# Kernel tuning notes

Measured on AMD Instinct MI355X. Metric: run time of the kernel, lower is better.

## Reference

```python
import math
import jax, jax.numpy as jnp
import numpy as np

B, C, L, EMB, ORDER = 4, 768, 8192, 33, 64


def setup_inputs() -> dict:
    key = jax.random.key(0)
    ks = jax.random.split(key, 8)
    x = jax.random.normal(ks[0], (B, C, L), jnp.float32)
    # 'batchias' param: jax.nn.initializers.normal() -> stddev 1e-2
    bias = 0.01 * jax.random.normal(ks[1], (C,), jnp.float32)
    # PositionalEmbedding z param (deterministic init)
    bands = (EMB - 1) // 2
    t_rescaled = jnp.linspace(0, L - 1, L)[None, :, None]
    w = 2 * math.pi * t_rescaled / L
    f = jnp.linspace(1e-4, bands - 1, bands)[None, None]
    zc = jnp.exp(-1j * f * w)
    time_emb = jnp.linspace(0, 1, L)[None, :, None]
    z = jnp.concatenate([time_emb, zc.real, zc.imag], axis=2).astype(jnp.float32)
    # ExponentialModulation deltas (deterministic init)
    target, fast_decay_pct, slow_decay_pct = 0.01, 0.3, 1.5
    max_decay = math.log(target) / fast_decay_pct
    min_decay = math.log(target) / slow_decay_pct
    deltas = jnp.linspace(min_decay, max_decay, C)[None, None].astype(jnp.float32)
    # implicit filter MLP params (Dense default lecun_normal-ish scale)
    def dense(k, fi, fo):
        return (jax.random.normal(k, (fi, fo), jnp.float32) / np.float32(np.sqrt(fi)))
    W0 = dense(ks[2], EMB, ORDER); b0 = jnp.zeros((ORDER,), jnp.float32)
    W1 = dense(ks[3], ORDER, ORDER); b1 = jnp.zeros((ORDER,), jnp.float32)
    W2 = dense(ks[4], ORDER, ORDER); b2 = jnp.zeros((ORDER,), jnp.float32)
    Wout = dense(ks[5], ORDER, C)  # no bias
    # Sin act constructed as Sin(dim=order) -> default freq=10, shared instance
    freq = 10.0 * jnp.ones((1, ORDER), jnp.float32)
    return dict(x=x, bias=bias, z=z, deltas=deltas, W0=W0, b0=b0, W1=W1, b1=b1,
                W2=W2, b2=b2, freq=freq, Wout=Wout, seq_len=L)


def _filter(z, deltas, W0, b0, W1, b1, W2, b2, freq, Wout, seq_len):
    # implicit MLP: (Dense -> Sin) x3, then Dense(num_channels, no bias)
    h = jnp.sin(freq * (z @ W0 + b0))
    h = jnp.sin(freq * (h @ W1 + b1))
    h = jnp.sin(freq * (h @ W2 + b2))
    h = h @ Wout  # [1, L, C]
    # exponential modulation: t = linspace(0,1,seq_len)
    t = jnp.linspace(0, 1, seq_len)[None, :, None]
    h = h * jnp.exp(-t * jnp.abs(deltas))
    return h


def _fft_conv(u, k, D):
    # u: [B, C, L], k: [C, L], D: [C]
    seq_len = u.shape[-1]
    fft_size = 2 * seq_len
    k_f = jnp.fft.rfft(k, n=fft_size) / fft_size
    u_f = jnp.fft.rfft(u, n=fft_size)
    y = jnp.fft.irfft(u_f * k_f, n=fft_size, norm='forward')[..., :seq_len]
    return (y + u * D[:, None]).astype(u.dtype)


def reference(x, bias, z, deltas, W0, b0, W1, b1, W2, b2, freq, Wout, seq_len):
    h = _filter(z, deltas, W0, b0, W1, b1, W2, b2, freq, Wout, seq_len)  # [1, L, C]
    k = h[0].T  # [C, L] (channel-major kernel as consumed by fft_conv)
    return _fft_conv(x, k, bias)
```

## Files before the change

### kernel.cpp

```cpp
#include <hip/hip_runtime.h>
#include <type_traits>
#include <utility>


typedef __attribute__((ext_vector_type(4))) short  short4v;
typedef __attribute__((ext_vector_type(8))) short  short8v;
typedef __attribute__((ext_vector_type(8))) __bf16 bf16x8;
typedef __attribute__((ext_vector_type(16))) float f32x16;

template <typename V, typename = void> struct MfmaTakes : std::false_type {};
template <typename V>
struct MfmaTakes<V, std::void_t<decltype(__builtin_amdgcn_mfma_f32_32x32x16_bf16(
    std::declval<V>(), std::declval<V>(), std::declval<f32x16>(), 0, 0, 0))>>
    : std::true_type {};

template <bool UseBf16> struct MfmaImpl;
template <> struct MfmaImpl<true> {
  template <typename V>
  static __device__ inline f32x16 run(V a, V b, f32x16 c) {
    return __builtin_amdgcn_mfma_f32_32x32x16_bf16(
        __builtin_bit_cast(bf16x8, a), __builtin_bit_cast(bf16x8, b), c, 0, 0, 0);
  }
};
template <> struct MfmaImpl<false> {
  template <typename V>
  static __device__ inline f32x16 run(V a, V b, f32x16 c) {
    return __builtin_amdgcn_mfma_f32_32x32x16_bf16(a, b, c, 0, 0, 0);
  }
};

__device__ inline f32x16 mfma_bf16(short8v a, short8v b, f32x16 c) {
  return MfmaImpl<MfmaTakes<bf16x8>::value>::run(a, b, c);
}

__device__ inline short8v pack8(short4v lo, short4v hi) {
  short8v v;
  v[0] = lo[0]; v[1] = lo[1]; v[2] = lo[2]; v[3] = lo[3];
  v[4] = hi[0]; v[5] = hi[1]; v[6] = hi[2]; v[7] = hi[3];
  return v;
}

__device__ inline short f2bf(float f) {
  unsigned int u = __builtin_bit_cast(unsigned int, f);
  u += 0x7FFFu + ((u >> 16) & 1u);
  return (short)(u >> 16);
}
__device__ inline float bf2f(short s) {
  unsigned int u = ((unsigned int)(unsigned short)s) << 16;
  return __builtin_bit_cast(float, u);
}

__device__ const unsigned char cGt[16]  = {2,7,4,6,1,7,4,6,5,7,3,6,3,0,5,5};
__device__ const short         cN0[16]  = {0,0,0,0,0,86,80,75,0,171,64,150,0,0,64,128};
__device__ const short         cN1[16]  = {96,86,80,75,64,171,160,150,64,256,128,224,64,32,128,192};
__device__ const unsigned char cSLOT[16]= {255,255,255,255,255,0,1,2,255,3,4,5,255,255,6,7};
__device__ const unsigned char cRA[16]  = {255,0,1,2,255,255,255,255,6,255,255,255,4,255,255,255};
__device__ const unsigned char cRB[16]  = {255,3,255,5,255,255,255,255,7,255,255,255,255,255,255,255};

__global__ __launch_bounds__(256) void hyena_filter(
    const float* __restrict__ z, const float* __restrict__ deltas,
    const float* __restrict__ W0, const float* __restrict__ b0,
    const float* __restrict__ W1, const float* __restrict__ b1,
    const float* __restrict__ W2, const float* __restrict__ b2,
    const float* __restrict__ freq, const float* __restrict__ Wout,
    short* __restrict__ gk) {
  __shared__ float zt[32][33];
  __shared__ __align__(16) float hA[32][64];
  __shared__ __align__(16) float hB[32][64];
  __shared__ __align__(16) unsigned int sT[256][20];
  const int tid = threadIdx.x;
  const int l0 = blockIdx.x << 5;

  for (int i = tid; i < 32 * 33; i += 256) {
    int l = i / 33, e = i - l * 33;
    zt[l][e] = z[(l0 + l) * 33 + e];
  }
  __syncthreads();
  for (int i = tid; i < 2048; i += 256) {
    int l = i >> 6, o = i & 63;
    float s = b0[o];
    for (int e = 0; e < 33; ++e) s += zt[l][e] * W0[e * 64 + o];
    hA[l][o] = sinf(freq[o] * s);
  }
  __syncthreads();
  for (int i = tid; i < 2048; i += 256) {
    int l = i >> 6, o = i & 63;
    float s = b1[o];
#pragma unroll
    for (int e = 0; e < 64; e += 4) {
      const float4 h4 = *reinterpret_cast<const float4*>(&hA[l][e]);
      s += h4.x * W1[e * 64 + o] + h4.y * W1[(e + 1) * 64 + o] +
           h4.z * W1[(e + 2) * 64 + o] + h4.w * W1[(e + 3) * 64 + o];
    }
    hB[l][o] = sinf(freq[o] * s);
  }
  __syncthreads();
  for (int i = tid; i < 2048; i += 256) {
    int l = i >> 6, o = i & 63;
    float s = b2[o];
#pragma unroll
    for (int e = 0; e < 64; e += 4) {
      const float4 h4 = *reinterpret_cast<const float4*>(&hB[l][e]);
      s += h4.x * W2[e * 64 + o] + h4.y * W2[(e + 1) * 64 + o] +
           h4.z * W2[(e + 2) * 64 + o] + h4.w * W2[(e + 3) * 64 + o];
    }
    hA[l][o] = sinf(freq[o] * s);
  }
  __syncthreads();
  {
    const int c0 = (blockIdx.y << 8) + tid;
    float a32[32];
#pragma unroll
    for (int l = 0; l < 32; ++l) a32[l] = 0.f;
    for (int o = 0; o < 64; o += 4) {
      const float w0 = Wout[(o + 0) * 768 + c0];
      const float w1 = Wout[(o + 1) * 768 + c0];
      const float w2 = Wout[(o + 2) * 768 + c0];
      const float w3 = Wout[(o + 3) * 768 + c0];
#pragma unroll
      for (int l = 0; l < 32; ++l) {
        const float4 h4 = *reinterpret_cast<const float4*>(&hA[l][o]);
        a32[l] += h4.x * w0 + h4.y * w1 + h4.z * w2 + h4.w * w3;
      }
    }
    const float del = fabsf(deltas[c0]);
#pragma unroll
    for (int l = 0; l < 32; ++l) {
      const float t = (float)(l0 + l) * (1.f / 8191.f);
      a32[l] *= expf(-t * del);
    }
#pragma unroll
    for (int d = 0; d < 16; ++d) {
      const unsigned int lo = (unsigned short)f2bf(a32[31 - 2 * d]);
      const unsigned int hi = (unsigned short)f2bf(a32[30 - 2 * d]);
      sT[tid][d] = lo | (hi << 16);
    }
  }
  __syncthreads();
  {
    const int lane = tid & 63, wid = tid >> 6;
    const int base_dw = 4080 - (blockIdx.x << 4);
    unsigned int* gku = reinterpret_cast<unsigned int*>(gk);
#pragma unroll
    for (int q = 0; q < 4; ++q) {
      const int r = (wid << 6) + (q << 4) + (lane >> 2);
      const int m = (lane & 3) << 2;
      const uint4 v = *reinterpret_cast<const uint4*>(&sT[r][m]);
      const size_t cg = (size_t)((blockIdx.y << 8) + r);
      *reinterpret_cast<uint4*>(gku + cg * 4096 + base_dw + m) = v;
    }
  }
}


#define ACC_ST(ACC, P, OFF)                                           \
  do {                                                                \
    _Pragma("unroll") for (int q = 0; q < 4; ++q) {                   \
      float4 v;                                                       \
      v.x = ACC[4 * q + 0]; v.y = ACC[4 * q + 1];                     \
      v.z = ACC[4 * q + 2]; v.w = ACC[4 * q + 3];                     \
      *reinterpret_cast<float4*>((P) + (OFF) + (q << 8)) = v;         \
    }                                                                 \
  } while (0)

#define ACC_LD(ACC, P, OFF)                                           \
  do {                                                                \
    _Pragma("unroll") for (int q = 0; q < 4; ++q) {                   \
      const float4 v =                                                \
          *reinterpret_cast<const float4*>((P) + (OFF) + (q << 8));   \
      ACC[4 * q + 0] += v.x; ACC[4 * q + 1] += v.y;                   \
      ACC[4 * q + 2] += v.z; ACC[4 * q + 3] += v.w;                   \
    }                                                                 \
  } while (0)

#define EPI(ACC, A)                                                   \
  do {                                                                \
    const int lb = lwb + ((A) << 8);                                  \
    _Pragma("unroll") for (int q = 0; q < 4; ++q) {                   \
      const int l0q = lb + (q << 3);                                  \
      const short4v xs =                                              \
          *reinterpret_cast<const short4v*>(&sXB[bcol][1008 + l0q]);  \
      float4 o4;                                                      \
      o4.x = ACC[4 * q + 0] + bc * bf2f(xs[0]);                       \
      o4.y = ACC[4 * q + 1] + bc * bf2f(xs[1]);                       \
      o4.z = ACC[4 * q + 2] + bc * bf2f(xs[2]);                       \
      o4.w = ACC[4 * q + 3] + bc * bf2f(xs[3]);                       \
      *reinterpret_cast<float4*>(out + obase + l0q) = o4;             \
    }                                                                 \
  } while (0)

__global__ __launch_bounds__(1024, 4) void hyena_conv(
    const float* __restrict__ x, const float* __restrict__ bias,
    const short* __restrict__ gk, float* __restrict__ out) {
  constexpr int LPAD = 1008;
  constexpr int XROW = 9224;
  __shared__ __align__(16) short sKR[4][8240];
  __shared__ __align__(16) short sXB[4][XROW];
  const int c = blockIdx.x;
  const int tid = threadIdx.x;

  {
    const short8v z8 = {0, 0, 0, 0, 0, 0, 0, 0};
    for (int b = 0; b < 4; ++b) {
      const float* xr = x + ((b * 768 + c) << 13);
      if (tid < 126)
        *reinterpret_cast<short8v*>(&sXB[b][tid << 3]) = z8;
      if (tid >= 1021)
        *reinterpret_cast<short8v*>(&sXB[b][9200 + ((tid - 1021) << 3)]) = z8;
      const int s0 = tid << 3;
      const float4 f0 = *reinterpret_cast<const float4*>(xr + s0);
      const float4 f1 = *reinterpret_cast<const float4*>(xr + s0 + 4);
      short8v v;
      v[0] = f2bf(f0.x); v[1] = f2bf(f0.y); v[2] = f2bf(f0.z); v[3] = f2bf(f0.w);
      v[4] = f2bf(f1.x); v[5] = f2bf(f1.y); v[6] = f2bf(f1.z); v[7] = f2bf(f1.w);
      *reinterpret_cast<short8v*>(&sXB[b][LPAD + s0]) = v;
    }
  }
  {
    const short* gkr = gk + (c << 13);
    for (int r = 0; r < 4; ++r)
      for (int u = tid; u < 8240; u += 1024) {
        int t = u + r;
        short v = 0;
        if (t >= 16 && t <= 8207) v = gkr[t - 16];
        sKR[r][u] = v;
      }
  }
  __syncthreads();

  const int lane = tid & 63;
  const int wid  = tid >> 6;
  const int i31  = lane & 31;
  const int half = lane >> 5;
  const int base = half << 3;
  const int tcol = i31 >> 2;
  const int bcol = i31 & 3;
  const float bc = bias[c];

  const int G    = cGt[wid];
  const int n0   = cN0[wid];
  const int n1   = cN1[wid];
  const int slot = cSLOT[wid];
  const int lbase = G << 10;

  const int af0 = 8207 - i31 + base;
  const int rho = af0 & 3;
  const int u00 = af0 & ~3;
  const int pb  = LPAD + lbase + (tcol << 5) + base;
  const int d0  = ((n0 >> 4) << 9) + ((n0 & 15) << 4);

  const short* ka = &sKR[rho][0] + (u00 + 16 - d0);
  const short* xa = &sXB[bcol][0] + (pb + 16 - d0);

  f32x16 acc0, acc1, acc2, acc3;
#pragma unroll
  for (int r = 0; r < 16; ++r) {
    acc0[r] = 0.f; acc1[r] = 0.f; acc2[r] = 0.f; acc3[r] = 0.f;
  }

#pragma unroll 2
  for (int n = n0; n < n1; ++n) {
    const short4v a0lo = *reinterpret_cast<const short4v*>(ka);
    const short4v a0hi = *reinterpret_cast<const short4v*>(ka + 4);
    const short4v a1lo = *reinterpret_cast<const short4v*>(ka - 256);
    const short4v a1hi = *reinterpret_cast<const short4v*>(ka - 252);
    const short8v A0 = pack8(a0lo, a0hi);
    const short8v A1 = pack8(a1lo, a1hi);
    const short8v Bm1 = *reinterpret_cast<const short8v*>(xa - 256);
    const short8v B0  = *reinterpret_cast<const short8v*>(xa);
    acc0 = mfma_bf16(A1, Bm1, acc0);
    acc0 = mfma_bf16(A0, B0, acc0);
    const short8v B1 = *reinterpret_cast<const short8v*>(xa + 256);
    acc1 = mfma_bf16(A1, B0, acc1);
    acc1 = mfma_bf16(A0, B1, acc1);
    const short8v B2 = *reinterpret_cast<const short8v*>(xa + 512);
    acc2 = mfma_bf16(A1, B1, acc2);
    acc2 = mfma_bf16(A0, B2, acc2);
    const short8v B3 = *reinterpret_cast<const short8v*>(xa + 768);
    acc3 = mfma_bf16(A1, B2, acc3);
    acc3 = mfma_bf16(A0, B3, acc3);
    const int dec = 16 + (((n & 15) == 15) << 8);
    ka -= dec; xa -= dec;
  }

  __syncthreads();
  float* scr = reinterpret_cast<float*>(&sKR[0][0]);
  const int isOwner = (slot == 255);
  float* sp = scr + (isOwner ? 0 : slot * 2048) + (lane << 2);
  const int ra = cRA[wid], rb = cRB[wid];
  if (!isOwner) { ACC_ST(acc0, sp, 0); ACC_ST(acc1, sp, 1024); }
  __syncthreads();
  if (isOwner) {
    if (ra != 255) {
      float* lp = scr + ra * 2048 + (lane << 2);
      ACC_LD(acc0, lp, 0); ACC_LD(acc1, lp, 1024);
    }
    if (rb != 255) {
      float* lp = scr + rb * 2048 + (lane << 2);
      ACC_LD(acc0, lp, 0); ACC_LD(acc1, lp, 1024);
    }
  }
  __syncthreads();
  if (!isOwner) { ACC_ST(acc2, sp, 0); ACC_ST(acc3, sp, 1024); }
  __syncthreads();
  if (isOwner) {
    if (ra != 255) {
      float* lp = scr + ra * 2048 + (lane << 2);
      ACC_LD(acc2, lp, 0); ACC_LD(acc3, lp, 1024);
    }
    if (rb != 255) {
      float* lp = scr + rb * 2048 + (lane << 2);
      ACC_LD(acc2, lp, 0); ACC_LD(acc3, lp, 1024);
    }
    const int obase = ((bcol * 768 + c) << 13);
    const int lwb = lbase + (tcol << 5) + (half << 2);
    EPI(acc0, 0); EPI(acc1, 1); EPI(acc2, 2); EPI(acc3, 3);
  }
}

extern "C" void kernel_launch(void* const* d_in, const int* in_sizes, int n_in,
                              void* d_out, int out_size, void* d_ws, size_t ws_size,
                              hipStream_t stream) {
  const float* x      = (const float*)d_in[0];
  const float* bias   = (const float*)d_in[1];
  const float* z      = (const float*)d_in[2];
  const float* deltas = (const float*)d_in[3];
  const float* W0     = (const float*)d_in[4];
  const float* b0     = (const float*)d_in[5];
  const float* W1     = (const float*)d_in[6];
  const float* b1     = (const float*)d_in[7];
  const float* W2     = (const float*)d_in[8];
  const float* b2     = (const float*)d_in[9];
  const float* freq   = (const float*)d_in[10];
  const float* Wout   = (const float*)d_in[11];
  float* out = (float*)d_out;
  short* gk = (short*)d_ws;

  hipLaunchKernelGGL(hyena_filter, dim3(256, 3), dim3(256), 0, stream,
                     z, deltas, W0, b0, W1, b1, W2, b2, freq, Wout, gk);
  hipLaunchKernelGGL(hyena_conv, dim3(768), dim3(1024), 0, stream,
                     x, bias, gk, out);
}
```

Before: 407.1 us.

## Split filter into MLP and Wout kernels; reorder conv MFMAs with setprio

The single filter kernel is split in two. One kernel computes the sine MLP once per position into a workspace buffer, and a second does the Wout projection with exponential modulation, writing the reversed bf16 kernel. This stops the MLP from being recomputed for each of the three channel groups and spreads the projection over more blocks. The conv inner loop now hoists all B loads ahead of the MFMAs, groups them by A operand and raises wave priority around them. The cost is an extra launch plus a global round trip for the hidden activations, and the new path only runs when the workspace is large enough.

```diff
diff --git a/kernel.cpp b/kernel.cpp
--- a/kernel.cpp
+++ b/kernel.cpp
@@ -57,7 +57,99 @@
 __device__ const unsigned char cRA[16]  = {255,0,1,2,255,255,255,255,6,255,255,255,4,255,255,255};
 __device__ const unsigned char cRB[16]  = {255,3,255,5,255,255,255,255,7,255,255,255,255,255,255,255};
 
-__global__ __launch_bounds__(256) void hyena_filter(
+__global__ __launch_bounds__(256) void hyena_mlp(
+    const float* __restrict__ z,
+    const float* __restrict__ W0, const float* __restrict__ b0,
+    const float* __restrict__ W1, const float* __restrict__ b1,
+    const float* __restrict__ W2, const float* __restrict__ b2,
+    const float* __restrict__ freq, float* __restrict__ h) {
+  __shared__ float zt[32][33];
+  __shared__ __align__(16) float hA[32][64];
+  __shared__ __align__(16) float hB[32][64];
+  const int tid = threadIdx.x;
+  const int l0 = blockIdx.x << 5;
+
+  for (int i = tid; i < 32 * 33; i += 256) {
+    int l = i / 33, e = i - l * 33;
+    zt[l][e] = z[(l0 + l) * 33 + e];
+  }
+  __syncthreads();
+  for (int i = tid; i < 2048; i += 256) {
+    int l = i >> 6, o = i & 63;
+    float s = b0[o];
+    for (int e = 0; e < 33; ++e) s += zt[l][e] * W0[e * 64 + o];
+    hA[l][o] = sinf(freq[o] * s);
+  }
+  __syncthreads();
+  for (int i = tid; i < 2048; i += 256) {
+    int l = i >> 6, o = i & 63;
+    float s = b1[o];
+#pragma unroll
+    for (int e = 0; e < 64; e += 4) {
+      const float4 h4 = *reinterpret_cast<const float4*>(&hA[l][e]);
+      s += h4.x * W1[e * 64 + o] + h4.y * W1[(e + 1) * 64 + o] +
+           h4.z * W1[(e + 2) * 64 + o] + h4.w * W1[(e + 3) * 64 + o];
+    }
+    hB[l][o] = sinf(freq[o] * s);
+  }
+  __syncthreads();
+  for (int i = tid; i < 2048; i += 256) {
+    int l = i >> 6, o = i & 63;
+    float s = b2[o];
+#pragma unroll
+    for (int e = 0; e < 64; e += 4) {
+      const float4 h4 = *reinterpret_cast<const float4*>(&hB[l][e]);
+      s += h4.x * W2[e * 64 + o] + h4.y * W2[(e + 1) * 64 + o] +
+           h4.z * W2[(e + 2) * 64 + o] + h4.w * W2[(e + 3) * 64 + o];
+    }
+    hA[l][o] = sinf(freq[o] * s);
+  }
+  __syncthreads();
+  for (int i = tid; i < 512; i += 256) {
+    const int l = i >> 4, o4 = (i & 15) << 2;
+    *reinterpret_cast<float4*>(h + ((l0 + l) << 6) + o4) =
+        *reinterpret_cast<const float4*>(&hA[l][o4]);
+  }
+}
+
+__global__ __launch_bounds__(256) void hyena_wout(
+    const float* __restrict__ h, const float* __restrict__ deltas,
+    const float* __restrict__ Wout, short* __restrict__ gk) {
+  const int tid = threadIdx.x;
+  const int c0 = (blockIdx.y << 8) + tid;
+  const int l0 = blockIdx.x << 4;
+  float a[16];
+#pragma unroll
+  for (int j = 0; j < 16; ++j) a[j] = 0.f;
+
+  const float* hb = h + ((size_t)l0 << 6);
+  for (int o = 0; o < 64; o += 4) {
+    const float w0 = Wout[(o + 0) * 768 + c0];
+    const float w1 = Wout[(o + 1) * 768 + c0];
+    const float w2 = Wout[(o + 2) * 768 + c0];
+    const float w3 = Wout[(o + 3) * 768 + c0];
+#pragma unroll
+    for (int j = 0; j < 16; ++j) {
+      const int off = __builtin_amdgcn_readfirstlane((j << 6) + o);
+      const float4 h4 = *reinterpret_cast<const float4*>(hb + off);
+      a[j] += h4.x * w0 + h4.y * w1 + h4.z * w2 + h4.w * w3;
+    }
+  }
+  const float del = fabsf(deltas[c0]);
+#pragma unroll
+  for (int j = 0; j < 16; ++j)
+    a[j] *= expf(-(float)(l0 + j) * (1.f / 8191.f) * del);
+
+  unsigned int* gku = reinterpret_cast<unsigned int*>(gk + ((size_t)c0 << 13));
+#pragma unroll
+  for (int j = 0; j < 16; j += 2) {
+    const unsigned int hi = (unsigned short)f2bf(a[j]);
+    const unsigned int lo = (unsigned short)f2bf(a[j + 1]);
+    gku[(8190 - l0 - j) >> 1] = lo | (hi << 16);
+  }
+}
+
+__global__ __launch_bounds__(256) void hyena_filter_mono(
     const float* __restrict__ z, const float* __restrict__ deltas,
     const float* __restrict__ W0, const float* __restrict__ b0,
     const float* __restrict__ W1, const float* __restrict__ b1,
@@ -268,17 +360,19 @@
     const short8v A1 = pack8(a1lo, a1hi);
     const short8v Bm1 = *reinterpret_cast<const short8v*>(xa - 256);
     const short8v B0  = *reinterpret_cast<const short8v*>(xa);
+    const short8v B1  = *reinterpret_cast<const short8v*>(xa + 256);
+    const short8v B2  = *reinterpret_cast<const short8v*>(xa + 512);
+    const short8v B3  = *reinterpret_cast<const short8v*>(xa + 768);
+    __builtin_amdgcn_s_setprio(1);
     acc0 = mfma_bf16(A1, Bm1, acc0);
+    acc1 = mfma_bf16(A1, B0, acc1);
+    acc2 = mfma_bf16(A1, B1, acc2);
+    acc3 = mfma_bf16(A1, B2, acc3);
     acc0 = mfma_bf16(A0, B0, acc0);
-    const short8v B1 = *reinterpret_cast<const short8v*>(xa + 256);
-    acc1 = mfma_bf16(A1, B0, acc1);
     acc1 = mfma_bf16(A0, B1, acc1);
-    const short8v B2 = *reinterpret_cast<const short8v*>(xa + 512);
-    acc2 = mfma_bf16(A1, B1, acc2);
     acc2 = mfma_bf16(A0, B2, acc2);
-    const short8v B3 = *reinterpret_cast<const short8v*>(xa + 768);
-    acc3 = mfma_bf16(A1, B2, acc3);
     acc3 = mfma_bf16(A0, B3, acc3);
+    __builtin_amdgcn_s_setprio(0);
     const int dec = 16 + (((n & 15) == 15) << 8);
     ka -= dec; xa -= dec;
   }
@@ -335,9 +429,19 @@
   const float* Wout   = (const float*)d_in[11];
   float* out = (float*)d_out;
   short* gk = (short*)d_ws;
-
-  hipLaunchKernelGGL(hyena_filter, dim3(256, 3), dim3(256), 0, stream,
-                     z, deltas, W0, b0, W1, b1, W2, b2, freq, Wout, gk);
+  const size_t GK_BYTES = (size_t)768 * 8192 * 2;
+  const size_t H_BYTES  = (size_t)8192 * 64 * 4;
+
+  if (ws_size >= GK_BYTES + H_BYTES) {
+    float* hbuf = (float*)((char*)d_ws + GK_BYTES);
+    hipLaunchKernelGGL(hyena_mlp, dim3(256), dim3(256), 0, stream,
+                       z, W0, b0, W1, b1, W2, b2, freq, hbuf);
+    hipLaunchKernelGGL(hyena_wout, dim3(512, 3), dim3(256), 0, stream,
+                       hbuf, deltas, Wout, gk);
+  } else {
+    hipLaunchKernelGGL(hyena_filter_mono, dim3(256, 3), dim3(256), 0, stream,
+                       z, deltas, W0, b0, W1, b1, W2, b2, freq, Wout, gk);
+  }
   hipLaunchKernelGGL(hyena_conv, dim3(768), dim3(1024), 0, stream,
                      x, bias, gk, out);
 }
```

After: 420.8 us. 3.3% more time.

## Widen conv MFMA inner step to four A fragments and shrink filter tiles

Applied to the files above, without the earlier changes.

The convolution inner loop now loads four kernel fragments (A0..A3) per step and issues sixteen MFMAs against shifted x fragments. It advances by 1024 per block of 16 steps instead of 512, so each warp takes fewer outer iterations with more register reuse of the loaded operands. The per-warp work-split tables are rebalanced for the new step size. The filter kernel now handles 16 positions per block over twice as many blocks and writes bf16 pairs straight to global memory, dropping the shared-memory transpose stage. That direct write pattern is less coalesced, and the wider loop raises register pressure.

```diff
diff --git a/kernel.cpp b/kernel.cpp
--- a/kernel.cpp
+++ b/kernel.cpp
@@ -50,12 +50,12 @@
   return __builtin_bit_cast(float, u);
 }
 
-__device__ const unsigned char cGt[16]  = {2,7,4,6,1,7,4,6,5,7,3,6,3,0,5,5};
-__device__ const short         cN0[16]  = {0,0,0,0,0,86,80,75,0,171,64,150,0,0,64,128};
-__device__ const short         cN1[16]  = {96,86,80,75,64,171,160,150,64,256,128,224,64,32,128,192};
-__device__ const unsigned char cSLOT[16]= {255,255,255,255,255,0,1,2,255,3,4,5,255,255,6,7};
-__device__ const unsigned char cRA[16]  = {255,0,1,2,255,255,255,255,6,255,255,255,4,255,255,255};
-__device__ const unsigned char cRB[16]  = {255,3,255,5,255,255,255,255,7,255,255,255,255,255,255,255};
+__device__ const unsigned char cGt[16]  = {0,1,2,3,7,3,5,6,7,4,5,6,7,4,5,6};
+__device__ const short         cN0[16]  = {0,0,0,0,0,32,0,0,43,0,32,38,86,40,64,75};
+__device__ const short         cN1[16]  = {16,32,48,32,43,64,32,38,86,40,64,75,128,80,96,112};
+__device__ const unsigned char cSLOT[16]= {255,255,255,255,255,0,255,255,1,255,2,3,4,5,6,7};
+__device__ const unsigned char cRA[16]  = {255,255,255,0,1,255,2,3,255,5,255,255,255,255,255,255};
+__device__ const unsigned char cRB[16]  = {255,255,255,255,4,255,6,7,255,255,255,255,255,255,255,255};
 
 __global__ __launch_bounds__(256) void hyena_filter(
     const float* __restrict__ z, const float* __restrict__ deltas,
@@ -64,26 +64,25 @@
     const float* __restrict__ W2, const float* __restrict__ b2,
     const float* __restrict__ freq, const float* __restrict__ Wout,
     short* __restrict__ gk) {
-  __shared__ float zt[32][33];
-  __shared__ __align__(16) float hA[32][64];
-  __shared__ __align__(16) float hB[32][64];
-  __shared__ __align__(16) unsigned int sT[256][20];
+  __shared__ float zt[16][33];
+  __shared__ __align__(16) float hA[16][64];
+  __shared__ __align__(16) float hB[16][64];
   const int tid = threadIdx.x;
-  const int l0 = blockIdx.x << 5;
-
-  for (int i = tid; i < 32 * 33; i += 256) {
+  const int l0 = blockIdx.x << 4;
+
+  for (int i = tid; i < 16 * 33; i += 256) {
     int l = i / 33, e = i - l * 33;
     zt[l][e] = z[(l0 + l) * 33 + e];
   }
   __syncthreads();
-  for (int i = tid; i < 2048; i += 256) {
+  for (int i = tid; i < 1024; i += 256) {
     int l = i >> 6, o = i & 63;
     float s = b0[o];
     for (int e = 0; e < 33; ++e) s += zt[l][e] * W0[e * 64 + o];
     hA[l][o] = sinf(freq[o] * s);
   }
   __syncthreads();
-  for (int i = tid; i < 2048; i += 256) {
+  for (int i = tid; i < 1024; i += 256) {
     int l = i >> 6, o = i & 63;
     float s = b1[o];
 #pragma unroll
@@ -95,7 +94,7 @@
     hB[l][o] = sinf(freq[o] * s);
   }
   __syncthreads();
-  for (int i = tid; i < 2048; i += 256) {
+  for (int i = tid; i < 1024; i += 256) {
     int l = i >> 6, o = i & 63;
     float s = b2[o];
 #pragma unroll
@@ -109,45 +108,31 @@
   __syncthreads();
   {
     const int c0 = (blockIdx.y << 8) + tid;
-    float a32[32];
-#pragma unroll
-    for (int l = 0; l < 32; ++l) a32[l] = 0.f;
+    float a[16];
+#pragma unroll
+    for (int j = 0; j < 16; ++j) a[j] = 0.f;
     for (int o = 0; o < 64; o += 4) {
       const float w0 = Wout[(o + 0) * 768 + c0];
       const float w1 = Wout[(o + 1) * 768 + c0];
       const float w2 = Wout[(o + 2) * 768 + c0];
       const float w3 = Wout[(o + 3) * 768 + c0];
 #pragma unroll
-      for (int l = 0; l < 32; ++l) {
-        const float4 h4 = *reinterpret_cast<const float4*>(&hA[l][o]);
-        a32[l] += h4.x * w0 + h4.y * w1 + h4.z * w2 + h4.w * w3;
+      for (int j = 0; j < 16; ++j) {
+        const float4 h4 = *reinterpret_cast<const float4*>(&hA[j][o]);
+        a[j] += h4.x * w0 + h4.y * w1 + h4.z * w2 + h4.w * w3;
       }
     }
     const float del = fabsf(deltas[c0]);
 #pragma unroll
-    for (int l = 0; l < 32; ++l) {
-      const float t = (float)(l0 + l) * (1.f / 8191.f);
-      a32[l] *= expf(-t * del);
-    }
-#pragma unroll
-    for (int d = 0; d < 16; ++d) {
-      const unsigned int lo = (unsigned short)f2bf(a32[31 - 2 * d]);
-      const unsigned int hi = (unsigned short)f2bf(a32[30 - 2 * d]);
-      sT[tid][d] = lo | (hi << 16);
-    }
-  }
-  __syncthreads();
-  {
-    const int lane = tid & 63, wid = tid >> 6;
-    const int base_dw = 4080 - (blockIdx.x << 4);
-    unsigned int* gku = reinterpret_cast<unsigned int*>(gk);
-#pragma unroll
-    for (int q = 0; q < 4; ++q) {
-      const int r = (wid << 6) + (q << 4) + (lane >> 2);
-      const int m = (lane & 3) << 2;
-      const uint4 v = *reinterpret_cast<const uint4*>(&sT[r][m]);
-      const size_t cg = (size_t)((blockIdx.y << 8) + r);
-      *reinterpret_cast<uint4*>(gku + cg * 4096 + base_dw + m) = v;
+    for (int j = 0; j < 16; ++j)
+      a[j] *= expf(-(float)(l0 + j) * (1.f / 8191.f) * del);
+
+    unsigned int* gku = reinterpret_cast<unsigned int*>(gk + ((size_t)c0 << 13));
+#pragma unroll
+    for (int j = 0; j < 16; j += 2) {
+      const unsigned int hi = (unsigned short)f2bf(a[j]);
+      const unsigned int lo = (unsigned short)f2bf(a[j + 1]);
+      gku[(8190 - l0 - j) >> 1] = lo | (hi << 16);
     }
   }
 }
@@ -247,7 +232,7 @@
   const int rho = af0 & 3;
   const int u00 = af0 & ~3;
   const int pb  = LPAD + lbase + (tcol << 5) + base;
-  const int d0  = ((n0 >> 4) << 9) + ((n0 & 15) << 4);
+  const int d0  = ((n0 >> 4) << 10) + ((n0 & 15) << 4);
 
   const short* ka = &sKR[rho][0] + (u00 + 16 - d0);
   const short* xa = &sXB[bcol][0] + (pb + 16 - d0);
@@ -260,26 +245,42 @@
 
 #pragma unroll 2
   for (int n = n0; n < n1; ++n) {
-    const short4v a0lo = *reinterpret_cast<const short4v*>(ka);
-    const short4v a0hi = *reinterpret_cast<const short4v*>(ka + 4);
-    const short4v a1lo = *reinterpret_cast<const short4v*>(ka - 256);
-    const short4v a1hi = *reinterpret_cast<const short4v*>(ka - 252);
-    const short8v A0 = pack8(a0lo, a0hi);
-    const short8v A1 = pack8(a1lo, a1hi);
+    const short4v lo0 = *reinterpret_cast<const short4v*>(ka);
+    const short4v hi0 = *reinterpret_cast<const short4v*>(ka + 4);
+    const short4v lo1 = *reinterpret_cast<const short4v*>(ka - 256);
+    const short4v hi1 = *reinterpret_cast<const short4v*>(ka - 252);
+    const short4v lo2 = *reinterpret_cast<const short4v*>(ka - 512);
+    const short4v hi2 = *reinterpret_cast<const short4v*>(ka - 508);
+    const short4v lo3 = *reinterpret_cast<const short4v*>(ka - 768);
+    const short4v hi3 = *reinterpret_cast<const short4v*>(ka - 764);
+    const short8v A0 = pack8(lo0, hi0);
+    const short8v A1 = pack8(lo1, hi1);
+    const short8v A2 = pack8(lo2, hi2);
+    const short8v A3 = pack8(lo3, hi3);
+    const short8v B0 = *reinterpret_cast<const short8v*>(xa);
+    const short8v B1 = *reinterpret_cast<const short8v*>(xa + 256);
+    const short8v B2 = *reinterpret_cast<const short8v*>(xa + 512);
+    const short8v B3 = *reinterpret_cast<const short8v*>(xa + 768);
+    acc0 = mfma_bf16(A0, B0, acc0);
+    acc1 = mfma_bf16(A0, B1, acc1);
+    acc2 = mfma_bf16(A0, B2, acc2);
+    acc3 = mfma_bf16(A0, B3, acc3);
     const short8v Bm1 = *reinterpret_cast<const short8v*>(xa - 256);
-    const short8v B0  = *reinterpret_cast<const short8v*>(xa);
     acc0 = mfma_bf16(A1, Bm1, acc0);
-    acc0 = mfma_bf16(A0, B0, acc0);
-    const short8v B1 = *reinterpret_cast<const short8v*>(xa + 256);
     acc1 = mfma_bf16(A1, B0, acc1);
-    acc1 = mfma_bf16(A0, B1, acc1);
-    const short8v B2 = *reinterpret_cast<const short8v*>(xa + 512);
     acc2 = mfma_bf16(A1, B1, acc2);
-    acc2 = mfma_bf16(A0, B2, acc2);
-    const short8v B3 = *reinterpret_cast<const short8v*>(xa + 768);
     acc3 = mfma_bf16(A1, B2, acc3);
-    acc3 = mfma_bf16(A0, B3, acc3);
-    const int dec = 16 + (((n & 15) == 15) << 8);
+    const short8v Bm2 = *reinterpret_cast<const short8v*>(xa - 512);
+    acc0 = mfma_bf16(A2, Bm2, acc0);
+    acc1 = mfma_bf16(A2, Bm1, acc1);
+    acc2 = mfma_bf16(A2, B0, acc2);
+    acc3 = mfma_bf16(A2, B1, acc3);
+    const short8v Bm3 = *reinterpret_cast<const short8v*>(xa - 768);
+    acc0 = mfma_bf16(A3, Bm3, acc0);
+    acc1 = mfma_bf16(A3, Bm2, acc1);
+    acc2 = mfma_bf16(A3, Bm1, acc2);
+    acc3 = mfma_bf16(A3, B0, acc3);
+    const int dec = ((n & 15) == 15) ? 784 : 16;
     ka -= dec; xa -= dec;
   }
 
@@ -336,7 +337,7 @@
   float* out = (float*)d_out;
   short* gk = (short*)d_ws;
 
-  hipLaunchKernelGGL(hyena_filter, dim3(256, 3), dim3(256), 0, stream,
+  hipLaunchKernelGGL(hyena_filter, dim3(512, 3), dim3(256), 0, stream,
                      z, deltas, W0, b0, W1, b1, W2, b2, freq, Wout, gk);
   hipLaunchKernelGGL(hyena_conv, dim3(768), dim3(1024), 0, stream,
                      x, bias, gk, out);
```

Result: no change. 408.2 us (+0.3%).
